# Kernel tuning notes

Hardware: AMD Instinct MI355X
Metric: run time of the kernel (lower is better)

## Reference

```python
import jax, jax.numpy as jnp
import numpy as np

_J6 = jnp.array([[0,0,0,0,0,1],[0,0,0,0,-1,0],[0,0,0,1,0,0],[0,0,1,0,0,0],[0,-1,0,0,0,0],[1,0,0,0,0,0]], dtype=jnp.float32)
# pairs (i,j) from combinations(range(4),2)
_PI = jnp.array([0,0,0,1,1,2])
_PJ = jnp.array([1,2,3,2,3,3])

def exterior(p1, p2):
    # p1, p2: [B,T,H,4] -> Plucker line coords [B,T,H,6], L2-normalized
    L = p1[..., _PI] * p2[..., _PJ] - p1[..., _PJ] * p2[..., _PI]
    n = jnp.clip(jnp.linalg.norm(L, axis=-1, keepdims=True), 1e-12)
    return L / n

def setup_inputs() -> dict:
    key = jax.random.key(0)
    ks = jax.random.split(key, 8)
    B, T, D, H = 2, 2048, 1024, 16
    pd = 4
    s = 0.02
    return {
        "x": jax.random.normal(ks[0], (B, T, D), jnp.float32),
        "w_qkv": jax.random.normal(ks[1], (3 * D, D), jnp.float32) * s,
        "b_qkv": jnp.zeros((3 * D,), jnp.float32),
        "w1_write": jax.random.normal(ks[2], (pd * H, D), jnp.float32) * s,
        "w2_write": jax.random.normal(ks[3], (pd * H, D), jnp.float32) * s,
        "w1_read": jax.random.normal(ks[4], (pd * H, D), jnp.float32) * s,
        "w2_read": jax.random.normal(ks[5], (pd * H, D), jnp.float32) * s,
        "w_out": jax.random.normal(ks[6], (D, D), jnp.float32) * s,
        "b_out": jnp.zeros((D,), jnp.float32),
        "decay_logits": jnp.full((H,), 4.6, jnp.float32),
        "bias_scale": jnp.full((H,), 0.1, jnp.float32),
    }

def reference(x, w_qkv, b_qkv, w1_write, w2_write, w1_read, w2_read, w_out, b_out, decay_logits, bias_scale):
    B, T, D = x.shape
    H = decay_logits.shape[0]
    dh = D // H
    pd = w1_write.shape[0] // H
    scale = dh ** -0.5

    qkv = (x @ w_qkv.T + b_qkv).reshape(B, T, 3, H, dh)
    qkv = jnp.transpose(qkv, (2, 0, 3, 1, 4))  # [3,B,H,T,dh]
    q, k, v = qkv[0], qkv[1], qkv[2]
    std_logits = jnp.einsum('bhqd,bhkd->bhqk', q, k) * scale

    x_prev = jnp.concatenate([jnp.zeros((B, 1, D), x.dtype), x[:, :-1]], axis=1)
    w1 = (x_prev @ w1_write.T).reshape(B, T, H, pd)
    w2 = (x @ w2_write.T).reshape(B, T, H, pd)
    write_lines = exterior(w1, w2)  # [B,T,H,6]
    r1 = (x @ w1_read.T).reshape(B, T, H, pd)
    r2 = (x @ w2_read.T).reshape(B, T, H, pd)
    read_lines = exterior(r1, r2)

    J_write = jnp.einsum('bthi,ij->bthj', write_lines, _J6)
    incidence = jnp.einsum('bqhp,bkhp->bhqk', read_lines, J_write)  # [B,H,T,T]

    decays = jax.nn.sigmoid(decay_logits)  # [H]
    pos = jnp.arange(T, dtype=x.dtype)
    diffs = pos[:, None] - pos[None, :]  # [T,T], q - k
    past = diffs > 0
    diffs_pos = jnp.where(past, diffs, 0.0)
    weights = (decays[:, None, None] ** diffs_pos[None]) * past[None].astype(x.dtype)  # [H,T,T]

    bias = incidence * weights[None] * bias_scale[None, :, None, None]
    logits = std_logits + bias
    causal_mask = diffs < 0  # k > q -> masked
    logits = jnp.where(causal_mask[None, None], -jnp.inf, logits)
    attn = jax.nn.softmax(logits, axis=-1)
    out = jnp.einsum('bhqk,bhkd->bqhd', attn, v).reshape(B, T, D)
    return out @ w_out.T + b_out
```

## Files before the change

kernel.cpp:

```cpp
#include <hip/hip_runtime.h>
#include <hip/hip_bf16.h>

using bhalf = __hip_bfloat16;
typedef __bf16 bf16x8 __attribute__((ext_vector_type(8)));
typedef __bf16 bf16x2 __attribute__((ext_vector_type(2)));
typedef float f32x4 __attribute__((ext_vector_type(4)));

#define B_DIM 2
#define T_DIM 2048
#define D_DIM 1024
#define H_DIM 16
#define DH 64

struct bh8 { bhalf v[8]; };
struct bh4 { bhalf v[4]; };

__device__ __forceinline__ bf16x8 load_bf16x8(const bhalf* p) {
    return __builtin_bit_cast(bf16x8, *(const uint4*)p);
}
__device__ __forceinline__ bf16x8 zero_bf16x8() {
    uint4 z; z.x = 0; z.y = 0; z.z = 0; z.w = 0;
    return __builtin_bit_cast(bf16x8, z);
}
__device__ __forceinline__ void stage8_cvt(bhalf* dst, const float* src) {
    float4 a = *(const float4*)src;
    float4 b = *(const float4*)(src + 4);
    bh8 t;
    t.v[0] = __float2bfloat16(a.x); t.v[1] = __float2bfloat16(a.y);
    t.v[2] = __float2bfloat16(a.z); t.v[3] = __float2bfloat16(a.w);
    t.v[4] = __float2bfloat16(b.x); t.v[5] = __float2bfloat16(b.y);
    t.v[6] = __float2bfloat16(b.z); t.v[7] = __float2bfloat16(b.w);
    *(uint4*)dst = __builtin_bit_cast(uint4, t);
}

#define GLD16(gp, lp) __builtin_amdgcn_global_load_lds( \
    (const __attribute__((address_space(1))) void*)(gp), \
    (__attribute__((address_space(3))) void*)(lp), 16, 0, 0)

#define SX  4194304
#define SW  3145728
#define SL  65536
#define SO  1048576
__global__ __launch_bounds__(256) void cvt_all(
    const float* __restrict__ x, const float* __restrict__ wqkv,
    const float* __restrict__ w1w, const float* __restrict__ w2w,
    const float* __restrict__ w1r, const float* __restrict__ w2r,
    const float* __restrict__ wout,
    bhalf* __restrict__ xbf, bhalf* __restrict__ wcat, bhalf* __restrict__ woutbf)
{
    int i = (blockIdx.x * 256 + threadIdx.x) * 8;
    if (i < SX) { stage8_cvt(xbf + i, x + i); return; }
    i -= SX;
    if (i < SW) { stage8_cvt(wcat + i, wqkv + i); return; }
    i -= SW;
    if (i < SL) { stage8_cvt(wcat + SW + i, w1w + i); return; }
    i -= SL;
    if (i < SL) { stage8_cvt(wcat + SW + SL + i, w2w + i); return; }
    i -= SL;
    if (i < SL) { stage8_cvt(wcat + SW + 2 * SL + i, w1r + i); return; }
    i -= SL;
    if (i < SL) { stage8_cvt(wcat + SW + 3 * SL + i, w2r + i); return; }
    i -= SL;
    if (i < SO) { stage8_cvt(woutbf + i, wout + i); }
}

__device__ __forceinline__ void gemm128_mainloop(
    const bhalf* __restrict__ A, const bhalf* __restrict__ B, int K,
    bhalf* As, bhalf* Bs, f32x4 acc[4][4])
{
    const int tid = threadIdx.x;
    const int wave = tid >> 6, lane = tid & 63;
    const int ln = lane & 15, lg = lane >> 4;
    const int wr = (wave >> 1) * 64, wc = (wave & 1) * 64;
    const int lrow = lane >> 3;
    const int lcol = (lane & 7) * 8;

    for (int kt = 0; kt < K; kt += 64) {
        __syncthreads();
#pragma unroll
        for (int i = 0; i < 4; ++i) {
            int idx = __builtin_amdgcn_readfirstlane(wave * 4 + i);
            GLD16(A + (size_t)(idx * 8 + lrow) * K + kt + lcol, As + idx * 512);
            GLD16(B + (size_t)(idx * 8 + lrow) * K + kt + lcol, Bs + idx * 512);
        }
        __syncthreads();
#pragma unroll
        for (int ks = 0; ks < 2; ++ks) {
            bf16x8 af[4], bfr[4];
#pragma unroll
            for (int mt = 0; mt < 4; ++mt)
                af[mt] = load_bf16x8(As + (wr + mt * 16 + ln) * 64 + ks * 32 + lg * 8);
#pragma unroll
            for (int nt = 0; nt < 4; ++nt)
                bfr[nt] = load_bf16x8(Bs + (wc + nt * 16 + ln) * 64 + ks * 32 + lg * 8);
#pragma unroll
            for (int mt = 0; mt < 4; ++mt)
#pragma unroll
                for (int nt = 0; nt < 4; ++nt)
                    acc[mt][nt] = __builtin_amdgcn_mfma_f32_16x16x32_bf16(af[mt], bfr[nt], acc[mt][nt], 0, 0, 0);
        }
    }
}

__global__ __launch_bounds__(256) void qkv_lines_gemm128(
    const bhalf* __restrict__ x, const bhalf* __restrict__ wcat, const float* __restrict__ bqkv,
    bhalf* __restrict__ qo, bhalf* __restrict__ ko, bhalf* __restrict__ vt,
    float* __restrict__ proj)
{
    __shared__ bhalf As[128 * 64];
    __shared__ bhalf Bs[128 * 64];
    f32x4 acc[4][4] = {};
    gemm128_mainloop(x + (size_t)blockIdx.x * 128 * D_DIM,
                     wcat + (size_t)blockIdx.y * 128 * D_DIM, D_DIM, As, Bs, acc);
    const int wave = threadIdx.x >> 6, lane = threadIdx.x & 63;
    const int ln = lane & 15, lg = lane >> 4;
    const int wr = (wave >> 1) * 64, wc = (wave & 1) * 64;
    const int trip = (blockIdx.y * 128) >> 10;

    if (trip == 2) {
#pragma unroll
        for (int nt = 0; nt < 4; ++nt) {
            int n = blockIdx.y * 128 + wc + nt * 16 + ln;
            float bias = bqkv[n];
            int h = (n >> 6) & 15, d = n & 63;
#pragma unroll
            for (int mt = 0; mt < 4; ++mt) {
                int tok0 = blockIdx.x * 128 + wr + mt * 16 + lg * 4;
                int b = tok0 >> 11, t0 = tok0 & (T_DIM - 1);
                bh4 pk;
#pragma unroll
                for (int r = 0; r < 4; ++r)
                    pk.v[r] = __float2bfloat16(acc[mt][nt][r] + bias);
                *(uint2*)&vt[(((size_t)(b * H_DIM + h)) * DH + d) * T_DIM + t0] =
                    __builtin_bit_cast(uint2, pk);
            }
        }
    } else {
#pragma unroll
        for (int nt = 0; nt < 4; ++nt) {
            int n = blockIdx.y * 128 + wc + nt * 16 + ln;
            int h = (n >> 6) & 15, d = n & 63;
            float bias = (trip < 3) ? bqkv[n] : 0.f;
#pragma unroll
            for (int mt = 0; mt < 4; ++mt)
#pragma unroll
                for (int r = 0; r < 4; ++r) {
                    int tok = blockIdx.x * 128 + wr + mt * 16 + lg * 4 + r;
                    int b = tok >> 11, t = tok & (T_DIM - 1);
                    float y = acc[mt][nt][r] + bias;
                    if (trip == 0) {
                        qo[(((size_t)(b * H_DIM + h)) * T_DIM + t) * DH + d] = __float2bfloat16(y * 0.125f);
                    } else if (trip == 1) {
                        ko[(((size_t)(b * H_DIM + h)) * T_DIM + t) * DH + d] = __float2bfloat16(y);
                    } else {
                        proj[(size_t)tok * 256 + (n - 3072)] = y;
                    }
                }
        }
    }
}

__global__ __launch_bounds__(256) void out_gemm64(
    const bhalf* __restrict__ a, const bhalf* __restrict__ w, const float* __restrict__ bo,
    float* __restrict__ out)
{
    __shared__ bhalf As[64 * 64];
    __shared__ bhalf Bs[64 * 64];
    const int tid = threadIdx.x;
    const int wave = tid >> 6, lane = tid & 63;
    const int ln = lane & 15, lg = lane >> 4;
    const int lrow = lane >> 3;
    const int lcol = (lane & 7) * 8;
    const bhalf* A = a + (size_t)blockIdx.x * 64 * D_DIM;
    const bhalf* B = w + (size_t)blockIdx.y * 64 * D_DIM;
    f32x4 acc[4] = {};

    for (int kt = 0; kt < D_DIM; kt += 64) {
        __syncthreads();
#pragma unroll
        for (int i = 0; i < 2; ++i) {
            int idx = __builtin_amdgcn_readfirstlane(wave * 2 + i);
            GLD16(A + (size_t)(idx * 8 + lrow) * D_DIM + kt + lcol, As + idx * 512);
            GLD16(B + (size_t)(idx * 8 + lrow) * D_DIM + kt + lcol, Bs + idx * 512);
        }
        __syncthreads();
#pragma unroll
        for (int ks = 0; ks < 2; ++ks) {
            bf16x8 af = load_bf16x8(As + (wave * 16 + ln) * 64 + ks * 32 + lg * 8);
#pragma unroll
            for (int nt = 0; nt < 4; ++nt) {
                bf16x8 bfr = load_bf16x8(Bs + (nt * 16 + ln) * 64 + ks * 32 + lg * 8);
                acc[nt] = __builtin_amdgcn_mfma_f32_16x16x32_bf16(af, bfr, acc[nt], 0, 0, 0);
            }
        }
    }
#pragma unroll
    for (int nt = 0; nt < 4; ++nt) {
        int n = blockIdx.y * 64 + nt * 16 + ln;
        float bias = bo[n];
#pragma unroll
        for (int r = 0; r < 4; ++r) {
            int tok = blockIdx.x * 64 + wave * 16 + lg * 4 + r;
            out[(size_t)tok * D_DIM + n] = acc[nt][r] + bias;
        }
    }
}

__global__ __launch_bounds__(256) void build_lines(
    const float* __restrict__ proj, const float* __restrict__ bias_scale,
    const float* __restrict__ decay_logits,
    bhalf* __restrict__ read8, bhalf* __restrict__ jw8)
{
    int id = blockIdx.x * 256 + threadIdx.x;
    int tok = id >> 4, h = id & 15;
    int b = tok >> 11, t = tok & (T_DIM - 1);
    const float* pr = proj + (size_t)tok * 256;

    float p1[4], p2[4], r1[4], r2[4];
#pragma unroll
    for (int i = 0; i < 4; ++i) {
        p1[i] = (t > 0) ? pr[-256 + h * 4 + i] : 0.f;
        p2[i] = pr[64 + h * 4 + i];
        r1[i] = pr[128 + h * 4 + i];
        r2[i] = pr[192 + h * 4 + i];
    }
    float Lw[6], Lr[6];
    {
        Lw[0] = p1[0] * p2[1] - p1[1] * p2[0];
        Lw[1] = p1[0] * p2[2] - p1[2] * p2[0];
        Lw[2] = p1[0] * p2[3] - p1[3] * p2[0];
        Lw[3] = p1[1] * p2[2] - p1[2] * p2[1];
        Lw[4] = p1[1] * p2[3] - p1[3] * p2[1];
        Lw[5] = p1[2] * p2[3] - p1[3] * p2[2];
        float n2 = 0.f;
#pragma unroll
        for (int j = 0; j < 6; ++j) n2 += Lw[j] * Lw[j];
        float inv = 1.f / fmaxf(sqrtf(n2), 1e-12f);
#pragma unroll
        for (int j = 0; j < 6; ++j) Lw[j] *= inv;
    }
    {
        Lr[0] = r1[0] * r2[1] - r1[1] * r2[0];
        Lr[1] = r1[0] * r2[2] - r1[2] * r2[0];
        Lr[2] = r1[0] * r2[3] - r1[3] * r2[0];
        Lr[3] = r1[1] * r2[2] - r1[2] * r2[1];
        Lr[4] = r1[1] * r2[3] - r1[3] * r2[1];
        Lr[5] = r1[2] * r2[3] - r1[3] * r2[2];
        float n2 = 0.f;
#pragma unroll
        for (int j = 0; j < 6; ++j) n2 += Lr[j] * Lr[j];
        float inv = 1.f / fmaxf(sqrtf(n2), 1e-12f);
#pragma unroll
        for (int j = 0; j < 6; ++j) Lr[j] *= inv;
    }
    float decay = 1.f / (1.f + __expf(-decay_logits[h]));
    float l2d = log2f(decay);
    float bs = bias_scale[h] * exp2f(-(float)t * l2d);
    size_t base = (((size_t)(b * H_DIM + h)) * T_DIM + t) * 8;
    read8[base + 0] = __float2bfloat16(Lr[0]);
    read8[base + 1] = __float2bfloat16(Lr[1]);
    read8[base + 2] = __float2bfloat16(Lr[2]);
    read8[base + 3] = __float2bfloat16(Lr[3]);
    read8[base + 4] = __float2bfloat16(Lr[4]);
    read8[base + 5] = __float2bfloat16(Lr[5]);
    read8[base + 6] = __float2bfloat16(0.f);
    read8[base + 7] = __float2bfloat16(0.f);
    jw8[base + 0] = __float2bfloat16(Lw[5] * bs);
    jw8[base + 1] = __float2bfloat16(-Lw[4] * bs);
    jw8[base + 2] = __float2bfloat16(Lw[3] * bs);
    jw8[base + 3] = __float2bfloat16(Lw[2] * bs);
    jw8[base + 4] = __float2bfloat16(-Lw[1] * bs);
    jw8[base + 5] = __float2bfloat16(Lw[0] * bs);
    jw8[base + 6] = __float2bfloat16(0.f);
    jw8[base + 7] = __float2bfloat16(0.f);
}

template<bool DIAG>
__device__ __forceinline__ void tile_step(
    const f32x4& z0, const f32x4& z1, const f32x4& i0, const f32x4& i1,
    int rq, int kb, const float* aq, int lg, int ln, bhalf* pl, float* lp)
{
    const float LOG2E = 1.44269504f;
#pragma unroll
    for (int r = 0; r < 4; ++r) {
        float p0, p1;
        if (DIAG) {
            int diff0 = rq + lg * 4 + r - (kb + 2 * ln);
            float s0 = z0[r] + ((diff0 > 0) ? i0[r] * aq[r] : 0.f);
            p0 = (diff0 < 0) ? 0.f : exp2f(s0 * LOG2E);
            int diff1 = diff0 - 1;
            float s1 = z1[r] + ((diff1 > 0) ? i1[r] * aq[r] : 0.f);
            p1 = (diff1 < 0) ? 0.f : exp2f(s1 * LOG2E);
        } else {
            p0 = exp2f(fmaf(i0[r], aq[r], z0[r]) * LOG2E);
            p1 = exp2f(fmaf(i1[r], aq[r], z1[r]) * LOG2E);
        }
        bf16x2 h2;
        h2.x = (__bf16)p0;
        h2.y = (__bf16)p1;
        *(unsigned int*)&pl[(lg * 4 + r) * 40 + 2 * ln] = __builtin_bit_cast(unsigned int, h2);
        lp[r] += p0 + p1;
    }
}

__global__ __launch_bounds__(256) void attn_kernel(
    const bhalf* __restrict__ q, const bhalf* __restrict__ k, const bhalf* __restrict__ vt,
    const bhalf* __restrict__ read8, const bhalf* __restrict__ jw8,
    const float* __restrict__ decay_logits, bhalf* __restrict__ attn_out)
{
    __shared__ float sm[4352];
    const int wave = threadIdx.x >> 6, lane = threadIdx.x & 63;
    const int ln = lane & 15, lg = lane >> 4;
    const int h = blockIdx.y, b = blockIdx.z;
    const int qa = blockIdx.x;
    const int qb = 127 - qa;
    const int rqa = qa * 16, rqb = qb * 16;
    const size_t hb = (size_t)(b * H_DIM + h);
    const bhalf* qh = q + hb * T_DIM * DH;
    const bhalf* kh = k + hb * T_DIM * DH;
    const bhalf* vh = vt + hb * DH * T_DIM;
    const bhalf* r8 = read8 + hb * T_DIM * 8;
    const bhalf* j8 = jw8 + hb * T_DIM * 8;

    bhalf* plA = (bhalf*)sm + wave * 640;
    bhalf* plB = (bhalf*)sm + 2560 + wave * 640;

    bf16x8 zf = zero_bf16x8();
    bf16x8 qA0 = load_bf16x8(qh + (rqa + ln) * DH + lg * 8);
    bf16x8 qA1 = load_bf16x8(qh + (rqa + ln) * DH + 32 + lg * 8);
    bf16x8 qB0 = load_bf16x8(qh + (rqb + ln) * DH + lg * 8);
    bf16x8 qB1 = load_bf16x8(qh + (rqb + ln) * DH + 32 + lg * 8);
    bf16x8 rfA = (lane < 16) ? load_bf16x8(r8 + (size_t)(rqa + ln) * 8) : zf;
    bf16x8 rfB = (lane < 16) ? load_bf16x8(r8 + (size_t)(rqb + ln) * 8) : zf;

    float decay = 1.f / (1.f + __expf(-decay_logits[h]));
    float l2d = log2f(decay);
    float aqA[4], aqB[4];
#pragma unroll
    for (int r = 0; r < 4; ++r) {
        aqA[r] = exp2f((float)(rqa + lg * 4 + r) * l2d);
        aqB[r] = exp2f((float)(rqb + lg * 4 + r) * l2d);
    }

    f32x4 oA[4] = {}, oB[4] = {};
    float lpA[4] = {0.f, 0.f, 0.f, 0.f}, lpB[4] = {0.f, 0.f, 0.f, 0.f};

    const int nca = qa / 2 + 1, ncb = qb / 2 + 1;
    for (int c = wave; c < ncb; c += 4) {
        const int kb = c * 32;
        bf16x8 k00 = load_bf16x8(kh + (kb + 2 * ln) * DH + lg * 8);
        bf16x8 k01 = load_bf16x8(kh + (kb + 2 * ln) * DH + 32 + lg * 8);
        bf16x8 k10 = load_bf16x8(kh + (kb + 2 * ln + 1) * DH + lg * 8);
        bf16x8 k11 = load_bf16x8(kh + (kb + 2 * ln + 1) * DH + 32 + lg * 8);
        bf16x8 j0 = (lane < 16) ? load_bf16x8(j8 + (size_t)(kb + 2 * ln) * 8) : zf;
        bf16x8 j1 = (lane < 16) ? load_bf16x8(j8 + (size_t)(kb + 2 * ln + 1) * 8) : zf;
        bf16x8 vf0 = load_bf16x8(vh + (size_t)(ln) * T_DIM + kb + lg * 8);
        bf16x8 vf1 = load_bf16x8(vh + (size_t)(16 + ln) * T_DIM + kb + lg * 8);
        bf16x8 vf2 = load_bf16x8(vh + (size_t)(32 + ln) * T_DIM + kb + lg * 8);
        bf16x8 vf3 = load_bf16x8(vh + (size_t)(48 + ln) * T_DIM + kb + lg * 8);
        const bool doA = (c < nca);

        {
            f32x4 z0 = {}, z1 = {}, i0 = {}, i1 = {};
            z0 = __builtin_amdgcn_mfma_f32_16x16x32_bf16(qB0, k00, z0, 0, 0, 0);
            z0 = __builtin_amdgcn_mfma_f32_16x16x32_bf16(qB1, k01, z0, 0, 0, 0);
            i0 = __builtin_amdgcn_mfma_f32_16x16x32_bf16(rfB, j0, i0, 0, 0, 0);
            z1 = __builtin_amdgcn_mfma_f32_16x16x32_bf16(qB0, k10, z1, 0, 0, 0);
            z1 = __builtin_amdgcn_mfma_f32_16x16x32_bf16(qB1, k11, z1, 0, 0, 0);
            i1 = __builtin_amdgcn_mfma_f32_16x16x32_bf16(rfB, j1, i1, 0, 0, 0);
            if (c == ncb - 1) tile_step<true >(z0, z1, i0, i1, rqb, kb, aqB, lg, ln, plB, lpB);
            else              tile_step<false>(z0, z1, i0, i1, rqb, kb, aqB, lg, ln, plB, lpB);
        }
        if (doA) {
            f32x4 z0 = {}, z1 = {}, i0 = {}, i1 = {};
            z0 = __builtin_amdgcn_mfma_f32_16x16x32_bf16(qA0, k00, z0, 0, 0, 0);
            z0 = __builtin_amdgcn_mfma_f32_16x16x32_bf16(qA1, k01, z0, 0, 0, 0);
            i0 = __builtin_amdgcn_mfma_f32_16x16x32_bf16(rfA, j0, i0, 0, 0, 0);
            z1 = __builtin_amdgcn_mfma_f32_16x16x32_bf16(qA0, k10, z1, 0, 0, 0);
            z1 = __builtin_amdgcn_mfma_f32_16x16x32_bf16(qA1, k11, z1, 0, 0, 0);
            i1 = __builtin_amdgcn_mfma_f32_16x16x32_bf16(rfA, j1, i1, 0, 0, 0);
            if (c == nca - 1) tile_step<true >(z0, z1, i0, i1, rqa, kb, aqA, lg, ln, plA, lpA);
            else              tile_step<false>(z0, z1, i0, i1, rqa, kb, aqA, lg, ln, plA, lpA);
        }
        __asm__ volatile("s_waitcnt lgkmcnt(0)" ::: "memory");
        {
            bf16x8 pf = load_bf16x8(plB + ln * 40 + lg * 8);
            oB[0] = __builtin_amdgcn_mfma_f32_16x16x32_bf16(pf, vf0, oB[0], 0, 0, 0);
            oB[1] = __builtin_amdgcn_mfma_f32_16x16x32_bf16(pf, vf1, oB[1], 0, 0, 0);
            oB[2] = __builtin_amdgcn_mfma_f32_16x16x32_bf16(pf, vf2, oB[2], 0, 0, 0);
            oB[3] = __builtin_amdgcn_mfma_f32_16x16x32_bf16(pf, vf3, oB[3], 0, 0, 0);
        }
        if (doA) {
            bf16x8 pf = load_bf16x8(plA + ln * 40 + lg * 8);
            oA[0] = __builtin_amdgcn_mfma_f32_16x16x32_bf16(pf, vf0, oA[0], 0, 0, 0);
            oA[1] = __builtin_amdgcn_mfma_f32_16x16x32_bf16(pf, vf1, oA[1], 0, 0, 0);
            oA[2] = __builtin_amdgcn_mfma_f32_16x16x32_bf16(pf, vf2, oA[2], 0, 0, 0);
            oA[3] = __builtin_amdgcn_mfma_f32_16x16x32_bf16(pf, vf3, oA[3], 0, 0, 0);
        }
    }

#pragma unroll
    for (int r = 0; r < 4; ++r) {
#pragma unroll
        for (int off = 1; off < 16; off <<= 1) {
            lpA[r] += __shfl_xor(lpA[r], off, 16);
            lpB[r] += __shfl_xor(lpB[r], off, 16);
        }
    }

    const int row = threadIdx.x >> 4;
    const int c4 = (threadIdx.x & 15) * 4;

    __syncthreads();
#pragma unroll
    for (int r = 0; r < 4; ++r) {
        if (ln == 0) sm[wave * 1088 + (lg * 4 + r) * 68 + 64] = lpA[r];
#pragma unroll
        for (int nt = 0; nt < 4; ++nt)
            sm[wave * 1088 + (lg * 4 + r) * 68 + nt * 16 + ln] = oA[nt][r];
    }
    __syncthreads();
    {
        float l = 0.f;
#pragma unroll
        for (int w = 0; w < 4; ++w) l += sm[w * 1088 + row * 68 + 64];
        float4 acc = {0.f, 0.f, 0.f, 0.f};
#pragma unroll
        for (int w = 0; w < 4; ++w) {
            float4 t = *(const float4*)&sm[w * 1088 + row * 68 + c4];
            acc.x += t.x; acc.y += t.y; acc.z += t.z; acc.w += t.w;
        }
        float invl = 1.f / l;
        bh4 pk;
        pk.v[0] = __float2bfloat16(acc.x * invl);
        pk.v[1] = __float2bfloat16(acc.y * invl);
        pk.v[2] = __float2bfloat16(acc.z * invl);
        pk.v[3] = __float2bfloat16(acc.w * invl);
        size_t tok = (size_t)b * T_DIM + rqa + row;
        *(uint2*)&attn_out[tok * D_DIM + h * DH + c4] = __builtin_bit_cast(uint2, pk);
    }

    __syncthreads();
#pragma unroll
    for (int r = 0; r < 4; ++r) {
        if (ln == 0) sm[wave * 1088 + (lg * 4 + r) * 68 + 64] = lpB[r];
#pragma unroll
        for (int nt = 0; nt < 4; ++nt)
            sm[wave * 1088 + (lg * 4 + r) * 68 + nt * 16 + ln] = oB[nt][r];
    }
    __syncthreads();
    {
        float l = 0.f;
#pragma unroll
        for (int w = 0; w < 4; ++w) l += sm[w * 1088 + row * 68 + 64];
        float4 acc = {0.f, 0.f, 0.f, 0.f};
#pragma unroll
        for (int w = 0; w < 4; ++w) {
            float4 t = *(const float4*)&sm[w * 1088 + row * 68 + c4];
            acc.x += t.x; acc.y += t.y; acc.z += t.z; acc.w += t.w;
        }
        float invl = 1.f / l;
        bh4 pk;
        pk.v[0] = __float2bfloat16(acc.x * invl);
        pk.v[1] = __float2bfloat16(acc.y * invl);
        pk.v[2] = __float2bfloat16(acc.z * invl);
        pk.v[3] = __float2bfloat16(acc.w * invl);
        size_t tok = (size_t)b * T_DIM + rqb + row;
        *(uint2*)&attn_out[tok * D_DIM + h * DH + c4] = __builtin_bit_cast(uint2, pk);
    }
}

extern "C" void kernel_launch(void* const* d_in, const int* in_sizes, int n_in,
                              void* d_out, int out_size, void* d_ws, size_t ws_size,
                              hipStream_t stream)
{
    const float* x    = (const float*)d_in[0];
    const float* wqkv = (const float*)d_in[1];
    const float* bqkv = (const float*)d_in[2];
    const float* w1w  = (const float*)d_in[3];
    const float* w2w  = (const float*)d_in[4];
    const float* w1r  = (const float*)d_in[5];
    const float* w2r  = (const float*)d_in[6];
    const float* wout = (const float*)d_in[7];
    const float* bout = (const float*)d_in[8];
    const float* dlog = (const float*)d_in[9];
    const float* bsc  = (const float*)d_in[10];
    float* out = (float*)d_out;

    char* ws = (char*)d_ws;
    bhalf* qb    = (bhalf*)(ws);
    bhalf* kbuf  = (bhalf*)(ws + 8388608);
    bhalf* vtb   = (bhalf*)(ws + 16777216);
    bhalf* r8    = (bhalf*)(ws + 25165824);
    bhalf* j8    = (bhalf*)(ws + 26214400);
    float* proj  = (float*)(ws + 27262976);
    bhalf* ao    = (bhalf*)(ws + 31457280);
    bhalf* woutbf = (bhalf*)(ws + 39845888);

    bhalf* xbf  = (bhalf*)d_out;
    bhalf* wcat = (bhalf*)((char*)d_out + 8388608);

    cvt_all<<<4224, 256, 0, stream>>>(x, wqkv, w1w, w2w, w1r, w2r, wout, xbf, wcat, woutbf);
    qkv_lines_gemm128<<<dim3(32, 26), 256, 0, stream>>>(xbf, wcat, bqkv, qb, kbuf, vtb, proj);
    build_lines<<<256, 256, 0, stream>>>(proj, bsc, dlog, r8, j8);
    attn_kernel<<<dim3(64, H_DIM, B_DIM), 256, 0, stream>>>(qb, kbuf, vtb, r8, j8, dlog, ao);
    out_gemm64<<<dim3(64, 16), 256, 0, stream>>>(ao, woutbf, bout, out);
}
```

Baseline: 302.6 us.

## Fuse line projections and Plucker build into prep kernel, convert w_out inline

Moves the small line-projection GEMM (x against the four write/read weights) and the Plucker line construction into the conversion kernel as extra blocks. Each block computes 15 tokens plus one halo row and writes read8/jw8 directly, which drops the fp32 proj buffer and a separate kernel launch. The out GEMM now reads fp32 w_out and converts it to bf16 in LDS, so the separate conversion pass is gone. Attention launch bounds gain a minimum of 6 blocks per CU. The trade-off is that the line blocks re-read weights redundantly, 274 times, and the out GEMM repeats its weight conversion in every block.

```diff
diff --git a/kernel.cpp b/kernel.cpp
--- a/kernel.cpp
+++ b/kernel.cpp
@@ -39,29 +39,130 @@
 
 #define SX  4194304
 #define SW  3145728
-#define SL  65536
-#define SO  1048576
-__global__ __launch_bounds__(256) void cvt_all(
+#define CVT_BLOCKS 3584
+#define LINES_BLOCKS 274
+
+__global__ __launch_bounds__(256) void prep(
     const float* __restrict__ x, const float* __restrict__ wqkv,
     const float* __restrict__ w1w, const float* __restrict__ w2w,
     const float* __restrict__ w1r, const float* __restrict__ w2r,
-    const float* __restrict__ wout,
-    bhalf* __restrict__ xbf, bhalf* __restrict__ wcat, bhalf* __restrict__ woutbf)
-{
-    int i = (blockIdx.x * 256 + threadIdx.x) * 8;
-    if (i < SX) { stage8_cvt(xbf + i, x + i); return; }
-    i -= SX;
-    if (i < SW) { stage8_cvt(wcat + i, wqkv + i); return; }
-    i -= SW;
-    if (i < SL) { stage8_cvt(wcat + SW + i, w1w + i); return; }
-    i -= SL;
-    if (i < SL) { stage8_cvt(wcat + SW + SL + i, w2w + i); return; }
-    i -= SL;
-    if (i < SL) { stage8_cvt(wcat + SW + 2 * SL + i, w1r + i); return; }
-    i -= SL;
-    if (i < SL) { stage8_cvt(wcat + SW + 3 * SL + i, w2r + i); return; }
-    i -= SL;
-    if (i < SO) { stage8_cvt(woutbf + i, wout + i); }
+    const float* __restrict__ bias_scale, const float* __restrict__ decay_logits,
+    bhalf* __restrict__ xbf, bhalf* __restrict__ wcat,
+    bhalf* __restrict__ read8, bhalf* __restrict__ jw8)
+{
+    __shared__ bhalf Bs[256 * 72];
+    __shared__ bhalf As[16 * 72];
+    const int tid = threadIdx.x;
+    const int bx = blockIdx.x;
+    if (bx < CVT_BLOCKS) {
+        int i = bx * 2048 + tid * 8;
+        if (i < SX) stage8_cvt(xbf + i, x + i);
+        else        stage8_cvt(wcat + (i - SX), wqkv + (i - SX));
+        return;
+    }
+    const int lb = bx - CVT_BLOCKS;
+    const int T0 = lb * 15;
+    const int wave = tid >> 6, lane = tid & 63;
+    const int ln = lane & 15, lg = lane >> 4;
+
+    const float* wsel = (tid < 64) ? w1w : (tid < 128) ? w2w : (tid < 192) ? w1r : w2r;
+    const float* brow = wsel + (size_t)(tid & 63) * D_DIM;
+
+    f32x4 acc[4] = {};
+    for (int kt = 0; kt < D_DIM; kt += 64) {
+        __syncthreads();
+        {
+            int r = tid >> 4;
+            int c4 = (tid & 15) * 4;
+            int tokrow = T0 - 1 + r;
+            tokrow = min(max(tokrow, 0), B_DIM * T_DIM - 1);
+            float4 a = *(const float4*)&x[(size_t)tokrow * D_DIM + kt + c4];
+            bh4 pk;
+            pk.v[0] = __float2bfloat16(a.x); pk.v[1] = __float2bfloat16(a.y);
+            pk.v[2] = __float2bfloat16(a.z); pk.v[3] = __float2bfloat16(a.w);
+            *(uint2*)&As[r * 72 + c4] = __builtin_bit_cast(uint2, pk);
+        }
+#pragma unroll
+        for (int c8 = 0; c8 < 64; c8 += 8)
+            stage8_cvt(&Bs[tid * 72 + c8], brow + kt + c8);
+        __syncthreads();
+#pragma unroll
+        for (int ks = 0; ks < 2; ++ks) {
+            bf16x8 af = load_bf16x8(&As[ln * 72 + ks * 32 + lg * 8]);
+#pragma unroll
+            for (int nt = 0; nt < 4; ++nt) {
+                bf16x8 bfr = load_bf16x8(&Bs[(wave * 64 + nt * 16 + ln) * 72 + ks * 32 + lg * 8]);
+                acc[nt] = __builtin_amdgcn_mfma_f32_16x16x32_bf16(af, bfr, acc[nt], 0, 0, 0);
+            }
+        }
+    }
+    float* smC = (float*)Bs;
+    __syncthreads();
+#pragma unroll
+    for (int nt = 0; nt < 4; ++nt)
+#pragma unroll
+        for (int r = 0; r < 4; ++r)
+            smC[(lg * 4 + r) * 260 + wave * 64 + nt * 16 + ln] = acc[nt][r];
+    __syncthreads();
+
+    int t_local = tid >> 4;
+    int h = tid & 15;
+    int token = T0 + t_local;
+    if (t_local < 15 && token < B_DIM * T_DIM) {
+        int t = token & (T_DIM - 1);
+        int b = token >> 11;
+        const float* prow  = &smC[(t_local + 1) * 260];
+        const float* pprev = &smC[t_local * 260];
+        float p1[4], p2[4], r1[4], r2[4];
+#pragma unroll
+        for (int i = 0; i < 4; ++i) {
+            p1[i] = (t > 0) ? pprev[h * 4 + i] : 0.f;
+            p2[i] = prow[64 + h * 4 + i];
+            r1[i] = prow[128 + h * 4 + i];
+            r2[i] = prow[192 + h * 4 + i];
+        }
+        float Lw[6], Lr[6];
+        Lw[0] = p1[0] * p2[1] - p1[1] * p2[0];
+        Lw[1] = p1[0] * p2[2] - p1[2] * p2[0];
+        Lw[2] = p1[0] * p2[3] - p1[3] * p2[0];
+        Lw[3] = p1[1] * p2[2] - p1[2] * p2[1];
+        Lw[4] = p1[1] * p2[3] - p1[3] * p2[1];
+        Lw[5] = p1[2] * p2[3] - p1[3] * p2[2];
+        float n2w = 0.f;
+#pragma unroll
+        for (int j = 0; j < 6; ++j) n2w += Lw[j] * Lw[j];
+        float invw = 1.f / fmaxf(sqrtf(n2w), 1e-12f);
+#pragma unroll
+        for (int j = 0; j < 6; ++j) Lw[j] *= invw;
+        Lr[0] = r1[0] * r2[1] - r1[1] * r2[0];
+        Lr[1] = r1[0] * r2[2] - r1[2] * r2[0];
+        Lr[2] = r1[0] * r2[3] - r1[3] * r2[0];
+        Lr[3] = r1[1] * r2[2] - r1[2] * r2[1];
+        Lr[4] = r1[1] * r2[3] - r1[3] * r2[1];
+        Lr[5] = r1[2] * r2[3] - r1[3] * r2[2];
+        float n2r = 0.f;
+#pragma unroll
+        for (int j = 0; j < 6; ++j) n2r += Lr[j] * Lr[j];
+        float invr = 1.f / fmaxf(sqrtf(n2r), 1e-12f);
+#pragma unroll
+        for (int j = 0; j < 6; ++j) Lr[j] *= invr;
+
+        float decay = 1.f / (1.f + __expf(-decay_logits[h]));
+        float l2d = log2f(decay);
+        float bs = bias_scale[h] * exp2f(-(float)t * l2d);
+        size_t base = (((size_t)(b * H_DIM + h)) * T_DIM + t) * 8;
+        bh8 ro, jo;
+        ro.v[0] = __float2bfloat16(Lr[0]); ro.v[1] = __float2bfloat16(Lr[1]);
+        ro.v[2] = __float2bfloat16(Lr[2]); ro.v[3] = __float2bfloat16(Lr[3]);
+        ro.v[4] = __float2bfloat16(Lr[4]); ro.v[5] = __float2bfloat16(Lr[5]);
+        ro.v[6] = __float2bfloat16(0.f);   ro.v[7] = __float2bfloat16(0.f);
+        *(uint4*)&read8[base] = __builtin_bit_cast(uint4, ro);
+        jo.v[0] = __float2bfloat16(Lw[5] * bs);  jo.v[1] = __float2bfloat16(-Lw[4] * bs);
+        jo.v[2] = __float2bfloat16(Lw[3] * bs);  jo.v[3] = __float2bfloat16(Lw[2] * bs);
+        jo.v[4] = __float2bfloat16(-Lw[1] * bs); jo.v[5] = __float2bfloat16(Lw[0] * bs);
+        jo.v[6] = __float2bfloat16(0.f);         jo.v[7] = __float2bfloat16(0.f);
+        *(uint4*)&jw8[base] = __builtin_bit_cast(uint4, jo);
+    }
 }
 
 __device__ __forceinline__ void gemm128_mainloop(
@@ -102,10 +203,9 @@
     }
 }
 
-__global__ __launch_bounds__(256) void qkv_lines_gemm128(
+__global__ __launch_bounds__(256) void qkv_gemm128(
     const bhalf* __restrict__ x, const bhalf* __restrict__ wcat, const float* __restrict__ bqkv,
-    bhalf* __restrict__ qo, bhalf* __restrict__ ko, bhalf* __restrict__ vt,
-    float* __restrict__ proj)
+    bhalf* __restrict__ qo, bhalf* __restrict__ ko, bhalf* __restrict__ vt)
 {
     __shared__ bhalf As[128 * 64];
     __shared__ bhalf Bs[128 * 64];
@@ -140,7 +240,7 @@
         for (int nt = 0; nt < 4; ++nt) {
             int n = blockIdx.y * 128 + wc + nt * 16 + ln;
             int h = (n >> 6) & 15, d = n & 63;
-            float bias = (trip < 3) ? bqkv[n] : 0.f;
+            float bias = bqkv[n];
 #pragma unroll
             for (int mt = 0; mt < 4; ++mt)
 #pragma unroll
@@ -150,10 +250,8 @@
                     float y = acc[mt][nt][r] + bias;
                     if (trip == 0) {
                         qo[(((size_t)(b * H_DIM + h)) * T_DIM + t) * DH + d] = __float2bfloat16(y * 0.125f);
-                    } else if (trip == 1) {
+                    } else {
                         ko[(((size_t)(b * H_DIM + h)) * T_DIM + t) * DH + d] = __float2bfloat16(y);
-                    } else {
-                        proj[(size_t)tok * 256 + (n - 3072)] = y;
                     }
                 }
         }
@@ -161,19 +259,22 @@
 }
 
 __global__ __launch_bounds__(256) void out_gemm64(
-    const bhalf* __restrict__ a, const bhalf* __restrict__ w, const float* __restrict__ bo,
+    const bhalf* __restrict__ a, const float* __restrict__ w, const float* __restrict__ bo,
     float* __restrict__ out)
 {
     __shared__ bhalf As[64 * 64];
-    __shared__ bhalf Bs[64 * 64];
+    __shared__ bhalf Bs[64 * 72];
     const int tid = threadIdx.x;
     const int wave = tid >> 6, lane = tid & 63;
     const int ln = lane & 15, lg = lane >> 4;
     const int lrow = lane >> 3;
     const int lcol = (lane & 7) * 8;
     const bhalf* A = a + (size_t)blockIdx.x * 64 * D_DIM;
-    const bhalf* B = w + (size_t)blockIdx.y * 64 * D_DIM;
+    const float* W = w + (size_t)blockIdx.y * 64 * D_DIM;
     f32x4 acc[4] = {};
+
+    const int br = tid >> 2;
+    const int bc = (tid & 3) * 16;
 
     for (int kt = 0; kt < D_DIM; kt += 64) {
         __syncthreads();
@@ -181,15 +282,16 @@
         for (int i = 0; i < 2; ++i) {
             int idx = __builtin_amdgcn_readfirstlane(wave * 2 + i);
             GLD16(A + (size_t)(idx * 8 + lrow) * D_DIM + kt + lcol, As + idx * 512);
-            GLD16(B + (size_t)(idx * 8 + lrow) * D_DIM + kt + lcol, Bs + idx * 512);
-        }
+        }
+        stage8_cvt(&Bs[br * 72 + bc], W + (size_t)br * D_DIM + kt + bc);
+        stage8_cvt(&Bs[br * 72 + bc + 8], W + (size_t)br * D_DIM + kt + bc + 8);
         __syncthreads();
 #pragma unroll
         for (int ks = 0; ks < 2; ++ks) {
             bf16x8 af = load_bf16x8(As + (wave * 16 + ln) * 64 + ks * 32 + lg * 8);
 #pragma unroll
             for (int nt = 0; nt < 4; ++nt) {
-                bf16x8 bfr = load_bf16x8(Bs + (nt * 16 + ln) * 64 + ks * 32 + lg * 8);
+                bf16x8 bfr = load_bf16x8(&Bs[(nt * 16 + ln) * 72 + ks * 32 + lg * 8]);
                 acc[nt] = __builtin_amdgcn_mfma_f32_16x16x32_bf16(af, bfr, acc[nt], 0, 0, 0);
             }
         }
@@ -204,75 +306,6 @@
             out[(size_t)tok * D_DIM + n] = acc[nt][r] + bias;
         }
     }
-}
-
-__global__ __launch_bounds__(256) void build_lines(
-    const float* __restrict__ proj, const float* __restrict__ bias_scale,
-    const float* __restrict__ decay_logits,
-    bhalf* __restrict__ read8, bhalf* __restrict__ jw8)
-{
-    int id = blockIdx.x * 256 + threadIdx.x;
-    int tok = id >> 4, h = id & 15;
-    int b = tok >> 11, t = tok & (T_DIM - 1);
-    const float* pr = proj + (size_t)tok * 256;
-
-    float p1[4], p2[4], r1[4], r2[4];
-#pragma unroll
-    for (int i = 0; i < 4; ++i) {
-        p1[i] = (t > 0) ? pr[-256 + h * 4 + i] : 0.f;
-        p2[i] = pr[64 + h * 4 + i];
-        r1[i] = pr[128 + h * 4 + i];
-        r2[i] = pr[192 + h * 4 + i];
-    }
-    float Lw[6], Lr[6];
-    {
-        Lw[0] = p1[0] * p2[1] - p1[1] * p2[0];
-        Lw[1] = p1[0] * p2[2] - p1[2] * p2[0];
-        Lw[2] = p1[0] * p2[3] - p1[3] * p2[0];
-        Lw[3] = p1[1] * p2[2] - p1[2] * p2[1];
-        Lw[4] = p1[1] * p2[3] - p1[3] * p2[1];
-        Lw[5] = p1[2] * p2[3] - p1[3] * p2[2];
-        float n2 = 0.f;
-#pragma unroll
-        for (int j = 0; j < 6; ++j) n2 += Lw[j] * Lw[j];
-        float inv = 1.f / fmaxf(sqrtf(n2), 1e-12f);
-#pragma unroll
-        for (int j = 0; j < 6; ++j) Lw[j] *= inv;
-    }
-    {
-        Lr[0] = r1[0] * r2[1] - r1[1] * r2[0];
-        Lr[1] = r1[0] * r2[2] - r1[2] * r2[0];
-        Lr[2] = r1[0] * r2[3] - r1[3] * r2[0];
-        Lr[3] = r1[1] * r2[2] - r1[2] * r2[1];
-        Lr[4] = r1[1] * r2[3] - r1[3] * r2[1];
-        Lr[5] = r1[2] * r2[3] - r1[3] * r2[2];
-        float n2 = 0.f;
-#pragma unroll
-        for (int j = 0; j < 6; ++j) n2 += Lr[j] * Lr[j];
-        float inv = 1.f / fmaxf(sqrtf(n2), 1e-12f);
-#pragma unroll
-        for (int j = 0; j < 6; ++j) Lr[j] *= inv;
-    }
-    float decay = 1.f / (1.f + __expf(-decay_logits[h]));
-    float l2d = log2f(decay);
-    float bs = bias_scale[h] * exp2f(-(float)t * l2d);
-    size_t base = (((size_t)(b * H_DIM + h)) * T_DIM + t) * 8;
-    read8[base + 0] = __float2bfloat16(Lr[0]);
-    read8[base + 1] = __float2bfloat16(Lr[1]);
-    read8[base + 2] = __float2bfloat16(Lr[2]);
-    read8[base + 3] = __float2bfloat16(Lr[3]);
-    read8[base + 4] = __float2bfloat16(Lr[4]);
-    read8[base + 5] = __float2bfloat16(Lr[5]);
-    read8[base + 6] = __float2bfloat16(0.f);
-    read8[base + 7] = __float2bfloat16(0.f);
-    jw8[base + 0] = __float2bfloat16(Lw[5] * bs);
-    jw8[base + 1] = __float2bfloat16(-Lw[4] * bs);
-    jw8[base + 2] = __float2bfloat16(Lw[3] * bs);
-    jw8[base + 3] = __float2bfloat16(Lw[2] * bs);
-    jw8[base + 4] = __float2bfloat16(-Lw[1] * bs);
-    jw8[base + 5] = __float2bfloat16(Lw[0] * bs);
-    jw8[base + 6] = __float2bfloat16(0.f);
-    jw8[base + 7] = __float2bfloat16(0.f);
 }
 
 template<bool DIAG>
@@ -303,7 +336,7 @@
     }
 }
 
-__global__ __launch_bounds__(256) void attn_kernel(
+__global__ __launch_bounds__(256, 6) void attn_kernel(
     const bhalf* __restrict__ q, const bhalf* __restrict__ k, const bhalf* __restrict__ vt,
     const bhalf* __restrict__ read8, const bhalf* __restrict__ jw8,
     const float* __restrict__ decay_logits, bhalf* __restrict__ attn_out)
@@ -493,16 +526,14 @@
     bhalf* vtb   = (bhalf*)(ws + 16777216);
     bhalf* r8    = (bhalf*)(ws + 25165824);
     bhalf* j8    = (bhalf*)(ws + 26214400);
-    float* proj  = (float*)(ws + 27262976);
-    bhalf* ao    = (bhalf*)(ws + 31457280);
-    bhalf* woutbf = (bhalf*)(ws + 39845888);
+    bhalf* ao    = (bhalf*)(ws + 27262976);
 
     bhalf* xbf  = (bhalf*)d_out;
     bhalf* wcat = (bhalf*)((char*)d_out + 8388608);
 
-    cvt_all<<<4224, 256, 0, stream>>>(x, wqkv, w1w, w2w, w1r, w2r, wout, xbf, wcat, woutbf);
-    qkv_lines_gemm128<<<dim3(32, 26), 256, 0, stream>>>(xbf, wcat, bqkv, qb, kbuf, vtb, proj);
-    build_lines<<<256, 256, 0, stream>>>(proj, bsc, dlog, r8, j8);
+    prep<<<CVT_BLOCKS + LINES_BLOCKS, 256, 0, stream>>>(
+        x, wqkv, w1w, w2w, w1r, w2r, bsc, dlog, xbf, wcat, r8, j8);
+    qkv_gemm128<<<dim3(32, 24), 256, 0, stream>>>(xbf, wcat, bqkv, qb, kbuf, vtb);
     attn_kernel<<<dim3(64, H_DIM, B_DIM), 256, 0, stream>>>(qb, kbuf, vtb, r8, j8, dlog, ao);
-    out_gemm64<<<dim3(64, 16), 256, 0, stream>>>(ao, woutbf, bout, out);
-}
+    out_gemm64<<<dim3(64, 16), 256, 0, stream>>>(ao, wout, bout, out);
+}
```

Measured after the change: 739.4 us. 144% more time.
